# Kernel optimization log

Hardware: AMD Instinct MI355X
Metric: run time of the kernel (lower is better)

The kernel has to match this reference:

```python
import jax, jax.numpy as jnp
import numpy as np


def pool_windows(a, k):
    # a: [..., H, W] with k == stride (non-overlapping windows)
    lead = a.shape[:-2]
    H, W = a.shape[-2], a.shape[-1]
    a = a.reshape(*lead, H // k, k, W // k, k)
    a = jnp.moveaxis(a, -3, -2)            # [..., Ho, Wo, k, k]
    return a.reshape(*lead, H // k, W // k, k * k)


def setup_inputs() -> dict:
    key = jax.random.key(0)
    k1, k2 = jax.random.split(key)
    S, C, H, W = 258, 64, 64, 64
    x = jax.random.normal(k1, (S, C, H, W), dtype=jnp.float32)
    # noise layer (last row) is nonnegative by convention
    x = x.at[-1].set(jnp.abs(x[-1]))
    x_true = jax.random.normal(k2, (C, H, W), dtype=jnp.float32)
    return {"x": x, "x_true": x_true, "kernel_size": 2, "stride": 2}


def reference(x, x_true, kernel_size, stride):
    # Zonotope/interval abstract transformer for MaxPool2d.
    # x: [S, C, H, W]; row 0 = center, rows 1:-1 = eps coeffs, row -1 = noise.
    assert kernel_size == stride
    k = kernel_size

    # Interval bounds per element (sum-of-abs reduction over symbol layers)
    eps_abs = jnp.sum(jnp.abs(x[1:]), axis=0)           # [C, H, W]
    lo = x[0] - eps_abs
    hi = x[0] + eps_abs

    xw = pool_windows(x, k)                              # [S, C, Ho, Wo, K]
    lw = pool_windows(lo, k)                             # [C, Ho, Wo, K]
    uw = pool_windows(hi, k)
    K = xw.shape[-1]

    # Candidate: window element with the largest lower bound
    i_star = jnp.argmax(lw, axis=-1)                     # [C, Ho, Wo]
    l_star = jnp.take_along_axis(lw, i_star[..., None], axis=-1)[..., 0]
    u_max = jnp.max(uw, axis=-1)

    # Max upper bound among the other window elements
    oh = jnp.arange(K) == i_star[..., None]              # one-hot of i_star
    u_other = jnp.max(jnp.where(oh, -jnp.inf, uw), axis=-1)

    # Exact case: the candidate dominates every other element -> pass its
    # affine form through. Otherwise fall back to the sound interval box
    # [l_star, u_max] (center +/- half-width in the noise layer).
    exact = l_star >= u_other                            # [C, Ho, Wo]

    gathered = jnp.take_along_axis(
        xw, i_star[None, ..., None], axis=-1)[..., 0]    # [S, C, Ho, Wo]

    box_center = 0.5 * (l_star + u_max)
    box_noise = 0.5 * (u_max - l_star)

    out_center = jnp.where(exact, gathered[0], box_center)
    out_eps = jnp.where(exact[None], gathered[1:-1], 0.0)
    out_noise = jnp.where(exact, jnp.abs(gathered[-1]), box_noise)

    x_out = jnp.concatenate(
        [out_center[None], out_eps, out_noise[None]], axis=0)

    out_abs = jnp.sum(jnp.abs(x_out[1:]), axis=0)
    x_min = x_out[0] - out_abs
    x_max = x_out[0] + out_abs

    x_true_out = jnp.max(pool_windows(x_true, k), axis=-1)
    return x_out, x_min, x_max, x_true_out
```

## Files before the change

### kernel.cpp

```cpp
#include <hip/hip_runtime.h>
#include <math.h>

#define S    258
#define C    64
#define H    64
#define W    64
#define HO   32
#define WO   32
#define NP   (C * HO * WO)
#define L    (C * H * W)
#define XOUT (S * NP)

__global__ __launch_bounds__(256) void k_main(const float* __restrict__ x,
                                              const float* __restrict__ x_true,
                                              float* __restrict__ out,
                                              int* __restrict__ counter,
                                              int2* __restrict__ exlist) {
    __shared__ float red[16][8][16];
    __shared__ float eps2[8][16];

    const int b   = blockIdx.x;
    const int c   = b >> 5;
    const int ho  = b & 31;
    const int tid = threadIdx.x;
    const int sg  = tid >> 4;
    const int wp  = tid & 15;

    const int rowbase = c * (H * W) + ho * 2 * W;
    const int A = rowbase + wp * 4;

    const int s0 = 1 + ((257 * sg) >> 4);
    const int s1 = 1 + ((257 * (sg + 1)) >> 4);

    float a0=0.f,a1=0.f,a2=0.f,a3=0.f,a4=0.f,a5=0.f,a6=0.f,a7=0.f;
    const float* px = x + (size_t)s0 * L + A;
    for (int s = s0; s < s1; ++s) {
        float4 t = *(const float4*)(px);
        float4 u = *(const float4*)(px + W);
        a0 += fabsf(t.x); a1 += fabsf(t.y); a2 += fabsf(t.z); a3 += fabsf(t.w);
        a4 += fabsf(u.x); a5 += fabsf(u.y); a6 += fabsf(u.z); a7 += fabsf(u.w);
        px += L;
    }
    red[sg][0][wp]=a0; red[sg][1][wp]=a1; red[sg][2][wp]=a2; red[sg][3][wp]=a3;
    red[sg][4][wp]=a4; red[sg][5][wp]=a5; red[sg][6][wp]=a6; red[sg][7][wp]=a7;
    __syncthreads();

    if (tid < 128) {
        const int e = tid >> 4, w = tid & 15;
        float sum = 0.f;
        #pragma unroll
        for (int j = 0; j < 16; ++j) sum += red[j][e][w];
        eps2[e][w] = sum;
    }
    __syncthreads();

    if (tid < 32) {
        const int wo  = tid;
        const int wq  = wo >> 1;
        const int odd = wo & 1;
        float eps[4];
        eps[0] = eps2[odd * 2 + 0][wq];
        eps[1] = eps2[odd * 2 + 1][wq];
        eps[2] = eps2[4 + odd * 2 + 0][wq];
        eps[3] = eps2[4 + odd * 2 + 1][wq];

        const int wbase = rowbase + wo * 2;
        float2 r0 = *(const float2*)(x + wbase);
        float2 r1 = *(const float2*)(x + wbase + W);
        float x0[4] = { r0.x, r0.y, r1.x, r1.y };
        float lo[4], hi[4];
        #pragma unroll
        for (int e = 0; e < 4; ++e) { lo[e] = x0[e] - eps[e]; hi[e] = x0[e] + eps[e]; }

        int istar = 0;
        #pragma unroll
        for (int e = 1; e < 4; ++e) if (lo[e] > lo[istar]) istar = e;

        const float lstar = lo[istar];
        const float umax  = fmaxf(fmaxf(hi[0], hi[1]), fmaxf(hi[2], hi[3]));
        float uoth = -INFINITY;
        #pragma unroll
        for (int e = 0; e < 4; ++e) if (e != istar) uoth = fmaxf(uoth, hi[e]);

        const bool exact = (lstar >= uoth);
        const int  pos   = wbase + (istar & 1) + (istar >> 1) * W;

        float center, noise;
        if (exact) {
            center = x0[istar];
            noise  = fabsf(x[(size_t)(S - 1) * L + pos]);
            int i  = atomicAdd(counter, 1);
            exlist[i] = make_int2(c * 1024 + ho * 32 + wo, pos);
        } else {
            center = 0.5f * (lstar + umax);
            noise  = 0.5f * (umax - lstar);
        }

        const int p = c * 1024 + ho * 32 + wo;
        out[p] = center;
        out[(size_t)(S - 1) * NP + p] = noise;
        out[XOUT + p] = lstar;
        out[XOUT + NP + p] = umax;

        float2 t0 = *(const float2*)(x_true + wbase);
        float2 t1 = *(const float2*)(x_true + wbase + W);
        out[XOUT + 2 * NP + p] = fmaxf(fmaxf(t0.x, t0.y), fmaxf(t1.x, t1.y));
    }
}

__global__ __launch_bounds__(256) void k_gather(const float* __restrict__ x,
                                                const int* __restrict__ counter,
                                                const int2* __restrict__ exlist,
                                                float* __restrict__ out) {
    const int n = counter[0];
    const int s = 1 + threadIdx.x;
    for (int i = blockIdx.x; i < n; i += gridDim.x) {
        const int2 e = exlist[i];
        out[(size_t)s * NP + e.x] = x[(size_t)s * L + e.y];
    }
}

extern "C" void kernel_launch(void* const* d_in, const int* in_sizes, int n_in,
                              void* d_out, int out_size, void* d_ws, size_t ws_size,
                              hipStream_t stream) {
    const float* x      = (const float*)d_in[0];
    const float* x_true = (const float*)d_in[1];
    float* out = (float*)d_out;

    int*  counter = (int*)d_ws;
    int2* exlist  = (int2*)((char*)d_ws + 256);

    hipMemsetAsync(out, 0, (size_t)XOUT * sizeof(float), stream);
    hipMemsetAsync(counter, 0, sizeof(int), stream);

    k_main<<<C * HO, 256, 0, stream>>>(x, x_true, out, counter, exlist);
    k_gather<<<64, 256, 0, stream>>>(x, counter, exlist, out);
}
```

Baseline: 393.7 us.

## Fuse memset, main pass and exact-gather into one kernel with shared-memory exact list

Removes the full-output memset and the separate gather kernel. Each block now zeroes only its own eps rows and keeps its exact outputs in a shared-memory list instead of a global atomic list, then copies the eps coefficients for those outputs itself. This drops two launches, the global atomic and a second dependent pass, at the cost of more serial work per block: strided zero stores and a loop over up to 32 gathers with one strided element per thread.

```diff
diff --git a/kernel.cpp b/kernel.cpp
--- a/kernel.cpp
+++ b/kernel.cpp
@@ -11,13 +11,14 @@
 #define L    (C * H * W)
 #define XOUT (S * NP)
 
-__global__ __launch_bounds__(256) void k_main(const float* __restrict__ x,
-                                              const float* __restrict__ x_true,
-                                              float* __restrict__ out,
-                                              int* __restrict__ counter,
-                                              int2* __restrict__ exlist) {
+__global__ __launch_bounds__(256) void k_fused(const float* __restrict__ x,
+                                               const float* __restrict__ x_true,
+                                               float* __restrict__ out) {
     __shared__ float red[16][8][16];
     __shared__ float eps2[8][16];
+    __shared__ int   ex_p[32];
+    __shared__ int   ex_pos[32];
+    __shared__ int   ex_n;
 
     const int b   = blockIdx.x;
     const int c   = b >> 5;
@@ -26,11 +27,20 @@
     const int sg  = tid >> 4;
     const int wp  = tid & 15;
 
+    if (tid == 0) ex_n = 0;
+
+    const int p0      = b * 32;
     const int rowbase = c * (H * W) + ho * 2 * W;
-    const int A = rowbase + wp * 4;
+
+    #pragma unroll 4
+    for (int i = tid; i < 256 * 32; i += 256) {
+        const int s = 1 + (i >> 5);
+        out[(size_t)s * NP + p0 + (i & 31)] = 0.0f;
+    }
 
     const int s0 = 1 + ((257 * sg) >> 4);
     const int s1 = 1 + ((257 * (sg + 1)) >> 4);
+    const int A  = rowbase + wp * 4;
 
     float a0=0.f,a1=0.f,a2=0.f,a3=0.f,a4=0.f,a5=0.f,a6=0.f,a7=0.f;
     const float* px = x + (size_t)s0 * L + A;
@@ -89,14 +99,15 @@
         if (exact) {
             center = x0[istar];
             noise  = fabsf(x[(size_t)(S - 1) * L + pos]);
-            int i  = atomicAdd(counter, 1);
-            exlist[i] = make_int2(c * 1024 + ho * 32 + wo, pos);
+            int i  = atomicAdd(&ex_n, 1);
+            ex_p[i]   = p0 + wo;
+            ex_pos[i] = pos;
         } else {
             center = 0.5f * (lstar + umax);
             noise  = 0.5f * (umax - lstar);
         }
 
-        const int p = c * 1024 + ho * 32 + wo;
+        const int p = p0 + wo;
         out[p] = center;
         out[(size_t)(S - 1) * NP + p] = noise;
         out[XOUT + p] = lstar;
@@ -106,17 +117,12 @@
         float2 t1 = *(const float2*)(x_true + wbase + W);
         out[XOUT + 2 * NP + p] = fmaxf(fmaxf(t0.x, t0.y), fmaxf(t1.x, t1.y));
     }
-}
+    __syncthreads();
 
-__global__ __launch_bounds__(256) void k_gather(const float* __restrict__ x,
-                                                const int* __restrict__ counter,
-                                                const int2* __restrict__ exlist,
-                                                float* __restrict__ out) {
-    const int n = counter[0];
-    const int s = 1 + threadIdx.x;
-    for (int i = blockIdx.x; i < n; i += gridDim.x) {
-        const int2 e = exlist[i];
-        out[(size_t)s * NP + e.x] = x[(size_t)s * L + e.y];
+    const int n = ex_n;
+    for (int j = 0; j < n; ++j) {
+        const int s = 1 + tid;
+        out[(size_t)s * NP + ex_p[j]] = x[(size_t)s * L + ex_pos[j]];
     }
 }
 
@@ -126,13 +132,5 @@
     const float* x      = (const float*)d_in[0];
     const float* x_true = (const float*)d_in[1];
     float* out = (float*)d_out;
-
-    int*  counter = (int*)d_ws;
-    int2* exlist  = (int2*)((char*)d_ws + 256);
-
-    hipMemsetAsync(out, 0, (size_t)XOUT * sizeof(float), stream);
-    hipMemsetAsync(counter, 0, sizeof(int), stream);
-
-    k_main<<<C * HO, 256, 0, stream>>>(x, x_true, out, counter, exlist);
-    k_gather<<<64, 256, 0, stream>>>(x, counter, exlist, out);
+    k_fused<<<C * HO, 256, 0, stream>>>(x, x_true, out);
 }
```

After: 386.2 us. About the same (-1.9%).
